# Performance work log

Measured on AMD Instinct MI355X. Metric: run time of the kernel, lower is better.

## Reference

```python
import jax, jax.numpy as jnp
import numpy as np

EMBED_DIM = 128
FFN_DIM = 512
N_NODES = 50000
N_EDGES = 800000
LN_EPS = 1e-5


def setup_inputs() -> dict:
    key = jax.random.key(0)
    ks = jax.random.split(key, 8)
    s = 1.0 / np.sqrt(EMBED_DIM)
    return {
        "x": jax.random.normal(ks[0], (N_NODES, EMBED_DIM), jnp.float32),
        "edge_indices": jax.random.randint(ks[1], (2, N_EDGES), 0, N_NODES, dtype=jnp.int32),
        "W_qkv": jax.random.normal(ks[2], (EMBED_DIM, 3 * EMBED_DIM), jnp.float32) * s,
        "b_qkv": jnp.zeros((3 * EMBED_DIM,), jnp.float32),
        "W1": jax.random.normal(ks[3], (EMBED_DIM, FFN_DIM), jnp.float32) * s,
        "b1": jnp.zeros((FFN_DIM,), jnp.float32),
        "W2": jax.random.normal(ks[4], (FFN_DIM, EMBED_DIM), jnp.float32) * (1.0 / np.sqrt(FFN_DIM)),
        "b2": jnp.zeros((EMBED_DIM,), jnp.float32),
        "g1": jnp.ones((EMBED_DIM,), jnp.float32),
        "be1": jnp.zeros((EMBED_DIM,), jnp.float32),
        "g2": jnp.ones((EMBED_DIM,), jnp.float32),
        "be2": jnp.zeros((EMBED_DIM,), jnp.float32),
    }


def _layernorm(x, g, b):
    mu = jnp.mean(x, axis=-1, keepdims=True)
    var = jnp.mean(jnp.square(x - mu), axis=-1, keepdims=True)
    return (x - mu) * jax.lax.rsqrt(var + LN_EPS) * g + b


def _self_attention(x, edge_indices, W_qkv, b_qkv):
    n = x.shape[0]
    scale = x.shape[1] ** (-0.5)
    qkv = x @ W_qkv + b_qkv
    q, k, v = jnp.split(qkv, 3, axis=1)
    src, dst = edge_indices[0], edge_indices[1]  # row (softmax segment), col
    # per-edge logits: [E]
    alpha = jnp.sum(q[src] * k[dst], axis=1) * scale
    # segment (per-row) stable softmax
    m = jax.ops.segment_max(alpha, src, num_segments=n)
    e = jnp.exp(alpha - m[src])
    denom = jax.ops.segment_sum(e, src, num_segments=n)
    w = e / denom[src]  # [E]
    # sparse.mm: out[i] = sum_{(i,j) in E} w_ij * v[j]
    return jax.ops.segment_sum(w[:, None] * v[dst], src, num_segments=n)


def reference(x, edge_indices, W_qkv, b_qkv, W1, b1, W2, b2, g1, be1, g2, be2):
    # norm_first = False (post-norm), dropout = 0
    x = _layernorm(x + _self_attention(x, edge_indices, W_qkv, b_qkv), g1, be1)
    h = jax.nn.relu(x @ W1 + b1) @ W2 + b2
    x = _layernorm(x + h, g2, be2)
    return x
```

## Files before the change

kernel.cpp:

```cpp
#include <hip/hip_runtime.h>
#include <math.h>

#define NN 50000
#define NE 800000
#define ED 128
#define FD 512
#define MAXDEG 64
#define QKV_BLOCKS (NN / 16)
#define SCAT_BLOCKS ((NE + 255) / 256)

typedef __attribute__((ext_vector_type(8))) short bf16x8;
typedef __attribute__((ext_vector_type(4))) float f32x4;
typedef _Float16 half2_t __attribute__((ext_vector_type(2)));

static __device__ __forceinline__ float wave_sum(float x) {
#pragma unroll
  for (int off = 32; off > 0; off >>= 1) x += __shfl_xor(x, off, 64);
  return x;
}

static __device__ __forceinline__ unsigned short f2bf(float f) {
  union { float f; unsigned u; } c; c.f = f;
  unsigned r = c.u + 0x7fffu + ((c.u >> 16) & 1u);
  return (unsigned short)(r >> 16);
}

static __device__ __forceinline__ unsigned short f2h(float f) {
  union { _Float16 h; unsigned short u; } c; c.h = (_Float16)f;
  return c.u;
}

static __device__ __forceinline__ half2_t u2h2(unsigned u) {
  union { unsigned u; half2_t h; } c; c.u = u;
  return c.h;
}

#if __has_builtin(__builtin_amdgcn_fdot2)
#define FDOT2(a, b, c) __builtin_amdgcn_fdot2((a), (b), (c), false)
#else
static __device__ __forceinline__ float FDOT2(half2_t a, half2_t b, float c) {
  return (float)a[0] * (float)b[0] + (float)a[1] * (float)b[1] + c;
}
#endif

__global__ void k_prep(const float* __restrict__ Wqkv, const float* __restrict__ W1,
                       const float* __restrict__ W2, unsigned short* __restrict__ WqkvF,
                       unsigned short* __restrict__ W1F, unsigned short* __restrict__ W2F,
                       int* __restrict__ cursor) {
  int idx = blockIdx.x * 256 + threadIdx.x;
  if (idx < NN) cursor[idx] = 0;
  if (idx < 49152) {
    int j = idx & 7, l = (idx >> 3) & 63, kb = (idx >> 9) & 3, t = idx >> 11;
    int k = kb * 32 + (l >> 4) * 8 + j, n = t * 16 + (l & 15);
    WqkvF[idx] = f2bf(Wqkv[k * 384 + n]);
  }
  {
    int j = idx & 7, l = (idx >> 3) & 63, kb = (idx >> 9) & 3, t = idx >> 11;
    int k = kb * 32 + (l >> 4) * 8 + j, n = t * 16 + (l & 15);
    W1F[idx] = f2bf(W1[k * 512 + n]);
  }
  {
    int j = idx & 7, l = (idx >> 3) & 63, kb = (idx >> 9) & 15, t = idx >> 13;
    int k = kb * 32 + (l >> 4) * 8 + j, n = t * 16 + (l & 15);
    W2F[idx] = f2bf(W2[k * 128 + n]);
  }
}

__global__ __launch_bounds__(256) void k_qkv(
    const float* __restrict__ X, const unsigned short* __restrict__ WqkvF,
    const float* __restrict__ B, unsigned short* __restrict__ q,
    unsigned short* __restrict__ kv) {
  __shared__ unsigned short xs[16][136];
  const int tid = threadIdx.x;
  const int row0 = blockIdx.x * 16;
  for (int idx = tid; idx < 512; idx += 256) {
    int r = idx >> 5, c4 = (idx & 31) << 2;
    float4 val = *(const float4*)&X[(size_t)(row0 + r) * ED + c4];
    xs[r][c4] = f2bf(val.x); xs[r][c4 + 1] = f2bf(val.y);
    xs[r][c4 + 2] = f2bf(val.z); xs[r][c4 + 3] = f2bf(val.w);
  }
  __syncthreads();
  const int wv = tid >> 6, lane = tid & 63;
  const int ln = lane & 15, quad = lane >> 4;
  const int koff = quad * 8;
  bf16x8 a[4];
#pragma unroll
  for (int kb = 0; kb < 4; kb++) a[kb] = *(const bf16x8*)&xs[ln][kb * 32 + koff];
  for (int g = 0; g < 3; g++) {
    const int t0 = wv * 6 + g * 2;
    bf16x8 b[2][4];
#pragma unroll
    for (int j = 0; j < 2; j++)
#pragma unroll
      for (int kb = 0; kb < 4; kb++)
        b[j][kb] = *(const bf16x8*)&WqkvF[(size_t)(((t0 + j) * 4 + kb) * 64 + lane) * 8];
    f32x4 acc[2];
#pragma unroll
    for (int j = 0; j < 2; j++) acc[j] = (f32x4){0.f, 0.f, 0.f, 0.f};
#pragma unroll
    for (int kb = 0; kb < 4; kb++)
#pragma unroll
      for (int j = 0; j < 2; j++)
        acc[j] = __builtin_amdgcn_mfma_f32_16x16x32_bf16(a[kb], b[j][kb], acc[j], 0, 0, 0);
#pragma unroll
    for (int j = 0; j < 2; j++) {
      const int col = (t0 + j) * 16 + ln;
      const float bias = B[col];
      if (col < 128) {
#pragma unroll
        for (int r = 0; r < 4; r++)
          q[(size_t)(row0 + quad * 4 + r) * ED + col] =
              f2h((acc[j][r] + bias) * 0.08838834764831845f);
      } else {
#pragma unroll
        for (int r = 0; r < 4; r++)
          kv[(size_t)(row0 + quad * 4 + r) * 256 + (col - 128)] = f2h(acc[j][r] + bias);
      }
    }
  }
}

__global__ __launch_bounds__(256) void k_scatter(
    const int* __restrict__ src, const int* __restrict__ dst,
    int* __restrict__ cursor, int* __restrict__ colidx) {
  const int e = blockIdx.x * 256 + threadIdx.x;
  if (e < NE) {
    const int s = src[e];
    const int d = dst[e];
    const int slot = atomicAdd(&cursor[s], 1);
    if (slot < MAXDEG) colidx[s * MAXDEG + slot] = d;
  }
}

template <bool FULL>
static __device__ __forceinline__ void attn_chunk(
    int base, int cnt, int grp, int gl, int lane, const half2_t* qh,
    const unsigned short* __restrict__ kv, const int* __restrict__ colidx,
    float& l, half2_t* axh) {
  const int C = FULL ? 16 : cnt;
  int colreg = 0;
  if (lane < C) colreg = colidx[base + lane];
  const int itmax = FULL ? 4 : ((C + 3) >> 2);
#pragma unroll(FULL ? 4 : 1)
  for (int it = 0; it < itmax; it++) {
    const int t = it * 4 + grp;
    const bool act = FULL || t < C;
    const int cc = __shfl(colreg, act ? t : 0, 64);
    const unsigned short* row = &kv[(size_t)cc * 256 + gl * 8];
    uint4 kw = *(const uint4*)row;
    uint4 vw = *(const uint4*)(row + 128);
    float dot = FDOT2(qh[0], u2h2(kw.x), 0.f);
    dot = FDOT2(qh[1], u2h2(kw.y), dot);
    dot = FDOT2(qh[2], u2h2(kw.z), dot);
    dot = FDOT2(qh[3], u2h2(kw.w), dot);
    dot += __shfl_xor(dot, 1, 64);
    dot += __shfl_xor(dot, 2, 64);
    dot += __shfl_xor(dot, 4, 64);
    dot += __shfl_xor(dot, 8, 64);
    const float e = act ? __expf(dot) : 0.f;
    l += e;
    const half2_t e2 = {(_Float16)e, (_Float16)e};
    axh[0] += e2 * u2h2(vw.x);
    axh[1] += e2 * u2h2(vw.y);
    axh[2] += e2 * u2h2(vw.z);
    axh[3] += e2 * u2h2(vw.w);
  }
}

__global__ __launch_bounds__(256) void k_attn(
    const unsigned short* __restrict__ q, const unsigned short* __restrict__ kv,
    const float* __restrict__ x, const int* __restrict__ cursor,
    const int* __restrict__ colidx, unsigned short* __restrict__ attb) {
  const int wv = threadIdx.x >> 6;
  const int lane = threadIdx.x & 63;
  const int grp = lane >> 4, gl = lane & 15;
  const int node = blockIdx.x * 4 + wv;

  half2_t qh[4];
  {
    uint4 qw = *(const uint4*)&q[(size_t)node * ED + gl * 8];
    qh[0] = u2h2(qw.x); qh[1] = u2h2(qw.y);
    qh[2] = u2h2(qw.z); qh[3] = u2h2(qw.w);
  }
  const int cnt0 = cursor[node];
  const int cnt = cnt0 > MAXDEG ? MAXDEG : cnt0;
  const int b0 = node * MAXDEG;
  float l = 0.f;
  half2_t axh[4] = {};
  int off = 0;
  for (; off + 16 <= cnt; off += 16)
    attn_chunk<true>(b0 + off, 16, grp, gl, lane, qh, kv, colidx, l, axh);
  if (off < cnt)
    attn_chunk<false>(b0 + off, cnt - off, grp, gl, lane, qh, kv, colidx, l, axh);

#pragma unroll
  for (int j = 0; j < 4; j++) {
    union { half2_t h; int i; } c;
    union { int i; half2_t h; } d;
    c.h = axh[j]; d.i = __shfl_xor(c.i, 16, 64); axh[j] += d.h;
    c.h = axh[j]; d.i = __shfl_xor(c.i, 32, 64); axh[j] += d.h;
  }
  l += __shfl_xor(l, 16, 64);
  l += __shfl_xor(l, 32, 64);

  const float inv = (cnt > 0) ? 1.0f / l : 0.f;
  const int d0 = gl * 8 + grp * 2;
  const half2_t s = (grp == 0) ? axh[0] : (grp == 1) ? axh[1] : (grp == 2) ? axh[2] : axh[3];
  float2 xv = *(const float2*)&x[(size_t)node * ED + d0];
  unsigned pk = (unsigned)f2h(xv.x + (float)s[0] * inv) |
                ((unsigned)f2h(xv.y + (float)s[1] * inv) << 16);
  *(unsigned*)&attb[(size_t)node * ED + d0] = pk;
}

__global__ __launch_bounds__(256) void k_ffn_ln2(
    const unsigned short* __restrict__ attb, const unsigned short* __restrict__ W1F,
    const float* __restrict__ b1, const unsigned short* __restrict__ W2F,
    const float* __restrict__ b2, const float* __restrict__ g1,
    const float* __restrict__ be1, const float* __restrict__ g2,
    const float* __restrict__ be2, float* __restrict__ out) {
  __shared__ unsigned short xs[16][136];
  __shared__ unsigned short hs[16][520];
  __shared__ float ysf[16][132];
  float* ys = (float*)&hs[0][0];
  const int row0 = blockIdx.x * 16;
  const int tid = threadIdx.x;
  {
    const int r = tid >> 4, c8 = (tid & 15) << 3;
    uint4 aw = *(const uint4*)&attb[(size_t)(row0 + r) * ED + c8];
    half2_t h0 = u2h2(aw.x), h1 = u2h2(aw.y), h2 = u2h2(aw.z), h3 = u2h2(aw.w);
    ysf[r][c8] = (float)h0[0];     ysf[r][c8 + 1] = (float)h0[1];
    ysf[r][c8 + 2] = (float)h1[0]; ysf[r][c8 + 3] = (float)h1[1];
    ysf[r][c8 + 4] = (float)h2[0]; ysf[r][c8 + 5] = (float)h2[1];
    ysf[r][c8 + 6] = (float)h3[0]; ysf[r][c8 + 7] = (float)h3[1];
  }
  __syncthreads();
  const int wv = tid >> 6, lane = tid & 63;
#pragma unroll
  for (int half = 0; half < 2; half++) {
    const int r = wv * 4 + half * 2 + (lane >> 5);
    const int hd = (lane & 31) << 2;
    float4 vv = *(const float4*)&ysf[r][hd];
    float s4 = vv.x + vv.y + vv.z + vv.w;
#pragma unroll
    for (int off = 16; off > 0; off >>= 1) s4 += __shfl_xor(s4, off, 64);
    const float mean = s4 * (1.f / ED);
    const float dx0 = vv.x - mean, dx1 = vv.y - mean, dx2 = vv.z - mean, dx3 = vv.w - mean;
    float vr = dx0 * dx0 + dx1 * dx1 + dx2 * dx2 + dx3 * dx3;
#pragma unroll
    for (int off = 16; off > 0; off >>= 1) vr += __shfl_xor(vr, off, 64);
    const float rstd = rsqrtf(vr * (1.f / ED) + 1e-5f);
    const float4 gg = *(const float4*)&g1[hd];
    const float4 bb = *(const float4*)&be1[hd];
    const float o0 = dx0 * rstd * gg.x + bb.x;
    const float o1 = dx1 * rstd * gg.y + bb.y;
    const float o2 = dx2 * rstd * gg.z + bb.z;
    const float o3 = dx3 * rstd * gg.w + bb.w;
    xs[r][hd] = f2bf(o0); xs[r][hd + 1] = f2bf(o1);
    xs[r][hd + 2] = f2bf(o2); xs[r][hd + 3] = f2bf(o3);
    *(float4*)&ysf[r][hd] = make_float4(o0, o1, o2, o3);
  }
  __syncthreads();
  const int ln = lane & 15, quad = lane >> 4;
  const int koff = quad * 8;
  bf16x8 a1[4];
#pragma unroll
  for (int kb = 0; kb < 4; kb++) a1[kb] = *(const bf16x8*)&xs[ln][kb * 32 + koff];
  for (int g = 0; g < 4; g++) {
    const int t0 = wv * 8 + g * 2;
    bf16x8 b[2][4];
#pragma unroll
    for (int j = 0; j < 2; j++)
#pragma unroll
      for (int kb = 0; kb < 4; kb++)
        b[j][kb] = *(const bf16x8*)&W1F[(size_t)(((t0 + j) * 4 + kb) * 64 + lane) * 8];
    f32x4 acc[2];
#pragma unroll
    for (int j = 0; j < 2; j++) acc[j] = (f32x4){0.f, 0.f, 0.f, 0.f};
#pragma unroll
    for (int kb = 0; kb < 4; kb++)
#pragma unroll
      for (int j = 0; j < 2; j++)
        acc[j] = __builtin_amdgcn_mfma_f32_16x16x32_bf16(a1[kb], b[j][kb], acc[j], 0, 0, 0);
#pragma unroll
    for (int j = 0; j < 2; j++) {
      const int col = (t0 + j) * 16 + ln;
      const float bias = b1[col];
#pragma unroll
      for (int r = 0; r < 4; r++)
        hs[quad * 4 + r][col] = f2bf(fmaxf(acc[j][r] + bias, 0.f));
    }
  }
  __syncthreads();
  f32x4 acc2[2];
  acc2[0] = (f32x4){0.f, 0.f, 0.f, 0.f};
  acc2[1] = (f32x4){0.f, 0.f, 0.f, 0.f};
  const int nt0 = wv * 2;
  for (int kg = 0; kg < 4; kg++) {
    bf16x8 a[4];
#pragma unroll
    for (int kk = 0; kk < 4; kk++)
      a[kk] = *(const bf16x8*)&hs[ln][(kg * 4 + kk) * 32 + koff];
    bf16x8 b[2][4];
#pragma unroll
    for (int nt = 0; nt < 2; nt++)
#pragma unroll
      for (int kk = 0; kk < 4; kk++)
        b[nt][kk] = *(const bf16x8*)&W2F[(size_t)(((nt0 + nt) * 16 + kg * 4 + kk) * 64 + lane) * 8];
#pragma unroll
    for (int kk = 0; kk < 4; kk++)
#pragma unroll
      for (int nt = 0; nt < 2; nt++)
        acc2[nt] = __builtin_amdgcn_mfma_f32_16x16x32_bf16(a[kk], b[nt][kk], acc2[nt], 0, 0, 0);
  }
  __syncthreads();
#pragma unroll
  for (int nt = 0; nt < 2; nt++) {
    const int col = (nt0 + nt) * 16 + ln;
    const float bias = b2[col];
#pragma unroll
    for (int r = 0; r < 4; r++)
      ys[(quad * 4 + r) * 132 + col] = acc2[nt][r] + bias;
  }
  __syncthreads();
  float2 gg = *(const float2*)&g2[2 * lane];
  float2 bbe = *(const float2*)&be2[2 * lane];
#pragma unroll
  for (int rr = 0; rr < 4; rr++) {
    const int r = wv * 4 + rr;
    const int row = row0 + r;
    float vx = ys[r * 132 + 2 * lane] + ysf[r][2 * lane];
    float vy = ys[r * 132 + 2 * lane + 1] + ysf[r][2 * lane + 1];
    float mean = wave_sum(vx + vy) * (1.f / ED);
    float dx = vx - mean, dy = vy - mean;
    float var = wave_sum(dx * dx + dy * dy) * (1.f / ED);
    float rstd = rsqrtf(var + 1e-5f);
    float2 o = make_float2(dx * rstd * gg.x + bbe.x, dy * rstd * gg.y + bbe.y);
    *(float2*)&out[(size_t)row * ED + 2 * lane] = o;
  }
}

extern "C" void kernel_launch(void* const* d_in, const int* in_sizes, int n_in,
                              void* d_out, int out_size, void* d_ws, size_t ws_size,
                              hipStream_t stream) {
  const float* x = (const float*)d_in[0];
  const int* ei = (const int*)d_in[1];
  const float* W_qkv = (const float*)d_in[2];
  const float* b_qkv = (const float*)d_in[3];
  const float* W1 = (const float*)d_in[4];
  const float* b1 = (const float*)d_in[5];
  const float* W2 = (const float*)d_in[6];
  const float* b2 = (const float*)d_in[7];
  const float* g1 = (const float*)d_in[8];
  const float* be1 = (const float*)d_in[9];
  const float* g2 = (const float*)d_in[10];
  const float* be2 = (const float*)d_in[11];
  float* out = (float*)d_out;

  char* ws = (char*)d_ws;
  size_t off = 0;
  auto alloc = [&](size_t bytes) -> char* {
    char* p = ws + off;
    off = (off + bytes + 255) & ~(size_t)255;
    return p;
  };
  unsigned short* q = (unsigned short*)alloc(2 * (size_t)NN * ED);
  unsigned short* kv = (unsigned short*)alloc(2 * (size_t)NN * 256);
  unsigned short* attb = (unsigned short*)alloc(2 * (size_t)NN * ED);
  unsigned short* WqkvF = (unsigned short*)alloc(2 * 24 * 4 * 64 * 8);
  unsigned short* W1F = (unsigned short*)alloc(2 * 32 * 4 * 64 * 8);
  unsigned short* W2F = (unsigned short*)alloc(2 * 8 * 16 * 64 * 8);
  int* cursor = (int*)alloc(sizeof(int) * NN);
  int* colidx = (int*)alloc(sizeof(int) * (size_t)NN * MAXDEG);

  k_prep<<<256, 256, 0, stream>>>(W_qkv, W1, W2, WqkvF, W1F, W2F, cursor);
  k_qkv<<<QKV_BLOCKS, 256, 0, stream>>>(x, WqkvF, b_qkv, q, kv);
  k_scatter<<<SCAT_BLOCKS, 256, 0, stream>>>(ei, ei + NE, cursor, colidx);
  k_attn<<<NN / 4, 256, 0, stream>>>(q, kv, x, cursor, colidx, attb);
  k_ffn_ln2<<<NN / 16, 256, 0, stream>>>(attb, W1F, b1, W2F, b2, g1, be1, g2, be2, out);
}
```

Measured before the change: 260.4 us.

## Merge QKV and edge scatter launches; double FFN rows per block for weight reuse

The edge-scatter kernel is folded into the QKV projection launch as extra blocks, so one launch is removed and the two independent jobs can run at the same time. The FFN+LayerNorm kernel now handles 32 rows per block instead of 16. Each W1/W2 fragment loaded from global memory feeds two MFMAs (low and high 16-row halves), which halves weight traffic per row. The cost is more shared memory and registers per block, which may lower occupancy, plus bounds checks for the partial last block.

```diff
diff --git a/kernel.cpp b/kernel.cpp
--- a/kernel.cpp
+++ b/kernel.cpp
@@ -8,6 +8,7 @@
 #define MAXDEG 64
 #define QKV_BLOCKS (NN / 16)
 #define SCAT_BLOCKS ((NE + 255) / 256)
+#define FFN_BLOCKS ((NN + 31) / 32)
 
 typedef __attribute__((ext_vector_type(8))) short bf16x8;
 typedef __attribute__((ext_vector_type(4))) float f32x4;
@@ -66,12 +67,24 @@
   }
 }
 
-__global__ __launch_bounds__(256) void k_qkv(
+__global__ __launch_bounds__(256) void k_qkv_scat(
     const float* __restrict__ X, const unsigned short* __restrict__ WqkvF,
     const float* __restrict__ B, unsigned short* __restrict__ q,
-    unsigned short* __restrict__ kv) {
+    unsigned short* __restrict__ kv, const int* __restrict__ src,
+    const int* __restrict__ dst, int* __restrict__ cursor,
+    int* __restrict__ colidx) {
   __shared__ unsigned short xs[16][136];
   const int tid = threadIdx.x;
+  if (blockIdx.x >= QKV_BLOCKS) {
+    const int e = (blockIdx.x - QKV_BLOCKS) * 256 + tid;
+    if (e < NE) {
+      const int s = src[e];
+      const int d = dst[e];
+      const int slot = atomicAdd(&cursor[s], 1);
+      if (slot < MAXDEG) colidx[s * MAXDEG + slot] = d;
+    }
+    return;
+  }
   const int row0 = blockIdx.x * 16;
   for (int idx = tid; idx < 512; idx += 256) {
     int r = idx >> 5, c4 = (idx & 31) << 2;
@@ -117,18 +130,6 @@
           kv[(size_t)(row0 + quad * 4 + r) * 256 + (col - 128)] = f2h(acc[j][r] + bias);
       }
     }
-  }
-}
-
-__global__ __launch_bounds__(256) void k_scatter(
-    const int* __restrict__ src, const int* __restrict__ dst,
-    int* __restrict__ cursor, int* __restrict__ colidx) {
-  const int e = blockIdx.x * 256 + threadIdx.x;
-  if (e < NE) {
-    const int s = src[e];
-    const int d = dst[e];
-    const int slot = atomicAdd(&cursor[s], 1);
-    if (slot < MAXDEG) colidx[s * MAXDEG + slot] = d;
   }
 }
 
@@ -218,26 +219,32 @@
     const float* __restrict__ b2, const float* __restrict__ g1,
     const float* __restrict__ be1, const float* __restrict__ g2,
     const float* __restrict__ be2, float* __restrict__ out) {
-  __shared__ unsigned short xs[16][136];
-  __shared__ unsigned short hs[16][520];
-  __shared__ float ysf[16][132];
+  __shared__ unsigned short xs[32][136];
+  __shared__ unsigned short hs[32][520];
+  __shared__ float ysf[32][132];
   float* ys = (float*)&hs[0][0];
-  const int row0 = blockIdx.x * 16;
+  const int row0 = blockIdx.x * 32;
   const int tid = threadIdx.x;
-  {
-    const int r = tid >> 4, c8 = (tid & 15) << 3;
-    uint4 aw = *(const uint4*)&attb[(size_t)(row0 + r) * ED + c8];
-    half2_t h0 = u2h2(aw.x), h1 = u2h2(aw.y), h2 = u2h2(aw.z), h3 = u2h2(aw.w);
-    ysf[r][c8] = (float)h0[0];     ysf[r][c8 + 1] = (float)h0[1];
-    ysf[r][c8 + 2] = (float)h1[0]; ysf[r][c8 + 3] = (float)h1[1];
-    ysf[r][c8 + 4] = (float)h2[0]; ysf[r][c8 + 5] = (float)h2[1];
-    ysf[r][c8 + 6] = (float)h3[0]; ysf[r][c8 + 7] = (float)h3[1];
+  for (int i = tid; i < 512; i += 256) {
+    const int r = i >> 4, c8 = (i & 15) << 3;
+    const int row = row0 + r;
+    if (row < NN) {
+      uint4 aw = *(const uint4*)&attb[(size_t)row * ED + c8];
+      half2_t h0 = u2h2(aw.x), h1 = u2h2(aw.y), h2 = u2h2(aw.z), h3 = u2h2(aw.w);
+      ysf[r][c8] = (float)h0[0];     ysf[r][c8 + 1] = (float)h0[1];
+      ysf[r][c8 + 2] = (float)h1[0]; ysf[r][c8 + 3] = (float)h1[1];
+      ysf[r][c8 + 4] = (float)h2[0]; ysf[r][c8 + 5] = (float)h2[1];
+      ysf[r][c8 + 6] = (float)h3[0]; ysf[r][c8 + 7] = (float)h3[1];
+    } else {
+#pragma unroll
+      for (int k = 0; k < 8; k++) ysf[r][c8 + k] = 0.f;
+    }
   }
   __syncthreads();
   const int wv = tid >> 6, lane = tid & 63;
 #pragma unroll
-  for (int half = 0; half < 2; half++) {
-    const int r = wv * 4 + half * 2 + (lane >> 5);
+  for (int pass = 0; pass < 4; pass++) {
+    const int r = wv * 8 + pass * 2 + (lane >> 5);
     const int hd = (lane & 31) << 2;
     float4 vv = *(const float4*)&ysf[r][hd];
     float s4 = vv.x + vv.y + vv.z + vv.w;
@@ -262,9 +269,12 @@
   __syncthreads();
   const int ln = lane & 15, quad = lane >> 4;
   const int koff = quad * 8;
-  bf16x8 a1[4];
-#pragma unroll
-  for (int kb = 0; kb < 4; kb++) a1[kb] = *(const bf16x8*)&xs[ln][kb * 32 + koff];
+  bf16x8 a1lo[4], a1hi[4];
+#pragma unroll
+  for (int kb = 0; kb < 4; kb++) {
+    a1lo[kb] = *(const bf16x8*)&xs[ln][kb * 32 + koff];
+    a1hi[kb] = *(const bf16x8*)&xs[16 + ln][kb * 32 + koff];
+  }
   for (int g = 0; g < 4; g++) {
     const int t0 = wv * 8 + g * 2;
     bf16x8 b[2][4];
@@ -273,33 +283,43 @@
 #pragma unroll
       for (int kb = 0; kb < 4; kb++)
         b[j][kb] = *(const bf16x8*)&W1F[(size_t)(((t0 + j) * 4 + kb) * 64 + lane) * 8];
-    f32x4 acc[2];
-#pragma unroll
-    for (int j = 0; j < 2; j++) acc[j] = (f32x4){0.f, 0.f, 0.f, 0.f};
+    f32x4 acc[2][2];
+#pragma unroll
+    for (int j = 0; j < 2; j++)
+#pragma unroll
+      for (int h = 0; h < 2; h++) acc[j][h] = (f32x4){0.f, 0.f, 0.f, 0.f};
 #pragma unroll
     for (int kb = 0; kb < 4; kb++)
 #pragma unroll
-      for (int j = 0; j < 2; j++)
-        acc[j] = __builtin_amdgcn_mfma_f32_16x16x32_bf16(a1[kb], b[j][kb], acc[j], 0, 0, 0);
+      for (int j = 0; j < 2; j++) {
+        acc[j][0] = __builtin_amdgcn_mfma_f32_16x16x32_bf16(a1lo[kb], b[j][kb], acc[j][0], 0, 0, 0);
+        acc[j][1] = __builtin_amdgcn_mfma_f32_16x16x32_bf16(a1hi[kb], b[j][kb], acc[j][1], 0, 0, 0);
+      }
 #pragma unroll
     for (int j = 0; j < 2; j++) {
       const int col = (t0 + j) * 16 + ln;
       const float bias = b1[col];
 #pragma unroll
-      for (int r = 0; r < 4; r++)
-        hs[quad * 4 + r][col] = f2bf(fmaxf(acc[j][r] + bias, 0.f));
-    }
-  }
-  __syncthreads();
-  f32x4 acc2[2];
-  acc2[0] = (f32x4){0.f, 0.f, 0.f, 0.f};
-  acc2[1] = (f32x4){0.f, 0.f, 0.f, 0.f};
+      for (int r = 0; r < 4; r++) {
+        hs[quad * 4 + r][col] = f2bf(fmaxf(acc[j][0][r] + bias, 0.f));
+        hs[16 + quad * 4 + r][col] = f2bf(fmaxf(acc[j][1][r] + bias, 0.f));
+      }
+    }
+  }
+  __syncthreads();
+  f32x4 acc2[2][2];
+#pragma unroll
+  for (int nt = 0; nt < 2; nt++)
+#pragma unroll
+    for (int h = 0; h < 2; h++) acc2[nt][h] = (f32x4){0.f, 0.f, 0.f, 0.f};
   const int nt0 = wv * 2;
   for (int kg = 0; kg < 4; kg++) {
-    bf16x8 a[4];
-#pragma unroll
-    for (int kk = 0; kk < 4; kk++)
-      a[kk] = *(const bf16x8*)&hs[ln][(kg * 4 + kk) * 32 + koff];
+    bf16x8 alo[4], ahi[4];
+#pragma unroll
+    for (int kk = 0; kk < 4; kk++) {
+      alo[kk] = *(const bf16x8*)&hs[ln][(kg * 4 + kk) * 32 + koff];
+      ahi[kk] = *(const bf16x8*)&hs[16 + ln][(kg * 4 + kk) * 32 + koff];
+    }
     bf16x8 b[2][4];
 #pragma unroll
     for (int nt = 0; nt < 2; nt++)
@@ -309,8 +329,10 @@
 #pragma unroll
     for (int kk = 0; kk < 4; kk++)
 #pragma unroll
-      for (int nt = 0; nt < 2; nt++)
-        acc2[nt] = __builtin_amdgcn_mfma_f32_16x16x32_bf16(a[kk], b[nt][kk], acc2[nt], 0, 0, 0);
+      for (int nt = 0; nt < 2; nt++) {
+        acc2[nt][0] = __builtin_amdgcn_mfma_f32_16x16x32_bf16(alo[kk], b[nt][kk], acc2[nt][0], 0, 0, 0);
+        acc2[nt][1] = __builtin_amdgcn_mfma_f32_16x16x32_bf16(ahi[kk], b[nt][kk], acc2[nt][1], 0, 0, 0);
+      }
   }
   __syncthreads();
 #pragma unroll
@@ -318,15 +340,17 @@
     const int col = (nt0 + nt) * 16 + ln;
     const float bias = b2[col];
 #pragma unroll
-    for (int r = 0; r < 4; r++)
-      ys[(quad * 4 + r) * 132 + col] = acc2[nt][r] + bias;
+    for (int r = 0; r < 4; r++) {
+      ys[(quad * 4 + r) * 132 + col] = acc2[nt][0][r] + bias;
+      ys[(16 + quad * 4 + r) * 132 + col] = acc2[nt][1][r] + bias;
+    }
   }
   __syncthreads();
   float2 gg = *(const float2*)&g2[2 * lane];
   float2 bbe = *(const float2*)&be2[2 * lane];
 #pragma unroll
-  for (int rr = 0; rr < 4; rr++) {
-    const int r = wv * 4 + rr;
+  for (int rr = 0; rr < 8; rr++) {
+    const int r = wv * 8 + rr;
     const int row = row0 + r;
     float vx = ys[r * 132 + 2 * lane] + ysf[r][2 * lane];
     float vy = ys[r * 132 + 2 * lane + 1] + ysf[r][2 * lane + 1];
@@ -334,8 +358,10 @@
     float dx = vx - mean, dy = vy - mean;
     float var = wave_sum(dx * dx + dy * dy) * (1.f / ED);
     float rstd = rsqrtf(var + 1e-5f);
-    float2 o = make_float2(dx * rstd * gg.x + bbe.x, dy * rstd * gg.y + bbe.y);
-    *(float2*)&out[(size_t)row * ED + 2 * lane] = o;
+    if (row < NN) {
+      float2 o = make_float2(dx * rstd * gg.x + bbe.x, dy * rstd * gg.y + bbe.y);
+      *(float2*)&out[(size_t)row * ED + 2 * lane] = o;
+    }
   }
 }
 
@@ -373,8 +399,8 @@
   int* colidx = (int*)alloc(sizeof(int) * (size_t)NN * MAXDEG);
 
   k_prep<<<256, 256, 0, stream>>>(W_qkv, W1, W2, WqkvF, W1F, W2F, cursor);
-  k_qkv<<<QKV_BLOCKS, 256, 0, stream>>>(x, WqkvF, b_qkv, q, kv);
-  k_scatter<<<SCAT_BLOCKS, 256, 0, stream>>>(ei, ei + NE, cursor, colidx);
+  k_qkv_scat<<<QKV_BLOCKS + SCAT_BLOCKS, 256, 0, stream>>>(x, WqkvF, b_qkv, q, kv,
+                                                           ei, ei + NE, cursor, colidx);
   k_attn<<<NN / 4, 256, 0, stream>>>(q, kv, x, cursor, colidx, attb);
-  k_ffn_ln2<<<NN / 16, 256, 0, stream>>>(attb, W1F, b1, W2F, b2, g1, be1, g2, be2, out);
-}
+  k_ffn_ln2<<<FFN_BLOCKS, 256, 0, stream>>>(attb, W1F, b1, W2F, b2, g1, be1, g2, be2, out);
+}
```

After: 279.1 us. 1.07x slower.
